# Kernel tuning notes

Measured on AMD Instinct MI355X. Metric: run time of the kernel, lower is better.

## Reference

```python
import jax, jax.numpy as jnp
import numpy as np

N = 8192      # total nodes (128 graphs x 64 electrodes)
L = 256       # signal_length
F = 64        # num_features
H = 128       # hidden_channels
G = 128       # num graphs
E = 262144    # num edges
C = 2         # n_classes


def setup_inputs() -> dict:
    key = jax.random.key(0)
    ks = jax.random.split(key, 20)
    def rn(k, shape, scale=0.05):
        return jax.random.normal(k, shape, jnp.float32) * scale
    return dict(
        x=jax.random.normal(ks[0], (N, L), jnp.float32),
        edge_index=jax.random.randint(ks[1], (2, E), 0, N),
        batch=jnp.repeat(jnp.arange(G), N // G),  # sorted graph id per node
        cw0=rn(ks[2], (F, 1, 7)), cb0=rn(ks[3], (F,)),
        cw_mid=rn(ks[4], (3, F, F, 5)), cb_mid=rn(ks[5], (3, F)),  # convs-2 = 3 middle convs
        cw_last=rn(ks[6], (F, F, 3)), cb_last=rn(ks[7], (F,)),
        enc_w=rn(ks[8], (F, F * 4)), enc_b=rn(ks[9], (F,)),  # in = F*((L-1)//2**6+1) = 256
        g0_rel_w=rn(ks[10], (H, F)), g0_rel_b=rn(ks[11], (H,)), g0_root_w=rn(ks[12], (H, F)),
        g_rel_w=rn(ks[13], (7, H, H)), g_rel_b=rn(ks[14], (7, H)), g_root_w=rn(ks[15], (7, H, H)),
        lin_w=rn(ks[16], (3, H, H)), lin_b=rn(ks[17], (3, H)),
        out_w=rn(ks[18], (C, H)), out_b=rn(ks[19], (C,)),
    )


def _conv1d(x, w, b, stride, pad):
    # x: [N, Cin, L], w: [Cout, Cin, K]
    y = jax.lax.conv_general_dilated(x, w, (stride,), [(pad, pad)],
                                     dimension_numbers=('NCH', 'OIH', 'NCH'))
    return y + b[None, :, None]


def reference(x, edge_index, batch, cw0, cb0, cw_mid, cb_mid, cw_last, cb_last,
              enc_w, enc_b, g0_rel_w, g0_rel_b, g0_root_w,
              g_rel_w, g_rel_b, g_root_w, lin_w, lin_b, out_w, out_b):
    act = jax.nn.relu
    rows = x.shape[0]
    h = x[:, None, :]                                    # [N, 1, L]
    h = act(_conv1d(h, cw0, cb0, 2, 3))                  # [N, F, L/2]
    for i in range(3):                                   # middle convs, k=5 s=2 p=2
        h = act(_conv1d(h, cw_mid[i], cb_mid[i], 2, 2))
    h = act(_conv1d(h, cw_last, cb_last, 2, 1))          # k=3 s=2 p=1 -> [N, F, 8]
    # AvgPool1d(k=3, s=2, p=1), count_include_pad=True -> always divide by 3
    h = jax.lax.reduce_window(h, 0.0, jax.lax.add, (1, 1, 3), (1, 1, 2),
                              [(0, 0), (0, 0), (1, 1)]) / 3.0   # [N, F, 4]
    h = h.reshape(rows, -1)                              # [N, F*4]
    h = h @ enc_w.T + enc_b                              # [N, F]
    src, dst = edge_index[0], edge_index[1]
    def gconv(h, rel_w, rel_b, root_w):
        # PyG GraphConv (aggr='add'): lin_rel(sum_j x_j) + lin_root(x)
        agg = jax.ops.segment_sum(h[src], dst, num_segments=N)
        return agg @ rel_w.T + rel_b + h @ root_w.T
    h = act(gconv(h, g0_rel_w, g0_rel_b, g0_root_w))     # hop 0: F -> H
    for i in range(7):                                   # hops 1..7: H -> H
        h = act(gconv(h, g_rel_w[i], g_rel_b[i], g_root_w[i]))
    # global mean pool by graph id
    sums = jax.ops.segment_sum(h, batch, num_segments=G)
    cnt = jax.ops.segment_sum(jnp.ones((N, 1), h.dtype), batch, num_segments=G)
    h = sums / jnp.maximum(cnt, 1.0)                     # [G, H]
    for i in range(3):
        h = act(h @ lin_w[i].T + lin_b[i])
    logits = h @ out_w.T + out_b                         # [G, C]
    return jax.nn.log_softmax(logits, -1)
```

## Files before the change

kernel.cpp:

```cpp
#include <hip/hip_runtime.h>
#include <hip/hip_bf16.h>

#define DEV_INLINE __device__ __forceinline__

typedef _Float16 f16;
typedef _Float16 f16x4 __attribute__((ext_vector_type(4)));
typedef _Float16 f16x8 __attribute__((ext_vector_type(8)));
typedef __bf16 bf16;
typedef __bf16 bf16x8 __attribute__((ext_vector_type(8)));
typedef float f32x16 __attribute__((ext_vector_type(16)));
typedef float f32x4 __attribute__((ext_vector_type(4)));

constexpr int N_NODES = 8192;
constexpr int G = 128;
constexpr int E_EDGES = 262144;


template<int MT, int LOG_PN, int IN_PS, int OUT_PS>
DEV_INLINE void conv_mid(const f16* __restrict__ wb, const float* __restrict__ bias,
                         char* inb, char* outb, int w, int l) {
  const int cht = w & 1;
  const int o_lane = cht * 32 + (l & 31);
  const int khalf = l >> 5;
  if ((w >> 1) < MT) {
    f16x8 wf[5][4];
#pragma unroll
    for (int k = 0; k < 5; k++)
#pragma unroll
      for (int s = 0; s < 4; s++)
        wf[k][s] = *(const f16x8*)&wb[(k * 64 + o_lane) * 64 + s * 16 + khalf * 8];
    f32x16 binit;
#pragma unroll
    for (int g = 0; g < 4; g++) {
      const float4 b4 = *(const float4*)&bias[cht * 32 + 8 * g + khalf * 4];
      binit[4 * g + 0] = b4.x; binit[4 * g + 1] = b4.y;
      binit[4 * g + 2] = b4.z; binit[4 * g + 3] = b4.w;
    }
    for (int mt = (w >> 1); mt < MT; mt += 2) {
      const int mo = mt * 32 + (l & 31);
      const int node = mo >> LOG_PN;
      const int po = mo & ((1 << LOG_PN) - 1);
      f32x16 acc = binit;
#pragma unroll
      for (int k = 0; k < 5; k++) {
        const int d = k - 2;
        const int par = d & 1;
        const int row = po + (d >> 1) + 1;
        const char* rb = inb + ((node * 2 + par) * IN_PS + row) * 128;
        const int fx = row & 7;
#pragma unroll
        for (int s = 0; s < 4; s++) {
          const int c8 = 2 * s + khalf;
          f16x8 af = *(const f16x8*)(rb + ((c8 ^ fx) << 4));
          acc = __builtin_amdgcn_mfma_f32_32x32x16_f16(wf[k][s], af, acc, 0, 0, 0);
        }
      }
      const int orow = (po >> 1) + 1;
      const int ofx = orow & 7;
      char* base = outb + ((node * 2 + (po & 1)) * OUT_PS + orow) * 128 + khalf * 8;
#pragma unroll
      for (int g = 0; g < 4; g++) {
        f16x4 h4;
        h4[0] = (f16)fmaxf(acc[4 * g + 0], 0.f);
        h4[1] = (f16)fmaxf(acc[4 * g + 1], 0.f);
        h4[2] = (f16)fmaxf(acc[4 * g + 2], 0.f);
        h4[3] = (f16)fmaxf(acc[4 * g + 3], 0.f);
        *(f16x4*)(base + (((cht * 4 + g) ^ ofx) << 4)) = h4;
      }
    }
  }
}

struct alignas(16) L12LDS {
  union {
    char act1[2][2][66][128];
    char a2s[16384];
  } A;
  f16 xs16[2][272];
};

__global__ __launch_bounds__(256)
__attribute__((amdgpu_waves_per_eu(4, 4)))
void conv_l1l2_kernel(
    const float* __restrict__ x,
    const f16* __restrict__ w0f, const float* __restrict__ cb0,
    const f16* __restrict__ wbmid, const float* __restrict__ cb_mid,
    f16* __restrict__ a2g) {
  __shared__ L12LDS lds;
  const int tid = threadIdx.x;
  const int w = tid >> 6, l = tid & 63;
  const int n0 = blockIdx.x * 2;

  for (int idx = tid; idx < 512; idx += 256) {
    int node = idx >> 8, j = idx & 255;
    lds.xs16[node][3 + j] = (f16)x[(size_t)(n0 + node) * 256 + j];
  }
  if (tid < 64) {
    int node = tid >> 5, t = tid & 31;
    int par = (t >> 3) & 1, hi = t >> 4, j = t & 7;
    *(int4*)&lds.A.act1[node][par][hi ? 65 : 0][j * 16] = make_int4(0, 0, 0, 0);
  } else if (tid < 96) {
    int t3 = tid - 64;
    int node = t3 >> 4, s = t3 & 15;
    int slot = (s < 3) ? s : (256 + s);
    lds.xs16[node][slot] = (f16)0.f;
  }
  __syncthreads();

  {
    const int cht = w & 1;
    const int o_lane = cht * 32 + (l & 31);
    const int khalf = l >> 5;
    const f16x8 w0frag = *(const f16x8*)&w0f[o_lane * 16 + khalf * 8];
    f32x16 binit;
#pragma unroll
    for (int g = 0; g < 4; g++) {
      const float4 b4 = *(const float4*)&cb0[cht * 32 + 8 * g + khalf * 4];
      binit[4 * g + 0] = b4.x; binit[4 * g + 1] = b4.y;
      binit[4 * g + 2] = b4.z; binit[4 * g + 3] = b4.w;
    }
    for (int mt = (w >> 1); mt < 8; mt += 2) {
      const int mo = mt * 32 + (l & 31);
      const int node = mo >> 7;
      const int po = mo & 127;
      union { uint u[4]; f16x8 v; } au;
      const char* ap = (const char*)&lds.xs16[node][2 * po + khalf * 8];
#pragma unroll
      for (int j = 0; j < 4; j++) au.u[j] = *(const uint*)(ap + 4 * j);
      f32x16 acc = __builtin_amdgcn_mfma_f32_32x32x16_f16(w0frag, au.v, binit, 0, 0, 0);
      const int orow = (po >> 1) + 1;
      const int ofx = orow & 7;
      char* base = (char*)lds.A.act1 + ((node * 2 + (po & 1)) * 66 + orow) * 128 + khalf * 8;
#pragma unroll
      for (int g = 0; g < 4; g++) {
        f16x4 h4;
        h4[0] = (f16)fmaxf(acc[4 * g + 0], 0.f);
        h4[1] = (f16)fmaxf(acc[4 * g + 1], 0.f);
        h4[2] = (f16)fmaxf(acc[4 * g + 2], 0.f);
        h4[3] = (f16)fmaxf(acc[4 * g + 3], 0.f);
        *(f16x4*)(base + (((cht * 4 + g) ^ ofx) << 4)) = h4;
      }
    }
  }
  __syncthreads();

  {
    const int cht = w & 1;
    const int o_lane = cht * 32 + (l & 31);
    const int khalf = l >> 5;
    f16x8 wf[5][4];
#pragma unroll
    for (int k = 0; k < 5; k++)
#pragma unroll
      for (int s = 0; s < 4; s++)
        wf[k][s] = *(const f16x8*)&wbmid[(k * 64 + o_lane) * 64 + s * 16 + khalf * 8];
    f32x16 binit;
#pragma unroll
    for (int g = 0; g < 4; g++) {
      const float4 b4 = *(const float4*)&cb_mid[cht * 32 + 8 * g + khalf * 4];
      binit[4 * g + 0] = b4.x; binit[4 * g + 1] = b4.y;
      binit[4 * g + 2] = b4.z; binit[4 * g + 3] = b4.w;
    }
    f16x4 outv[2][4];
#pragma unroll
    for (int it = 0; it < 2; it++) {
      const int mt = (w >> 1) + it * 2;
      const int mo = mt * 32 + (l & 31);
      const int node = mo >> 6;
      const int po = mo & 63;
      f32x16 acc = binit;
#pragma unroll
      for (int k = 0; k < 5; k++) {
        const int d = k - 2;
        const int par = d & 1;
        const int row = po + (d >> 1) + 1;
        const char* rb = (char*)lds.A.act1 + ((node * 2 + par) * 66 + row) * 128;
        const int fx = row & 7;
#pragma unroll
        for (int s = 0; s < 4; s++) {
          const int c8 = 2 * s + khalf;
          f16x8 af = *(const f16x8*)(rb + ((c8 ^ fx) << 4));
          acc = __builtin_amdgcn_mfma_f32_32x32x16_f16(wf[k][s], af, acc, 0, 0, 0);
        }
      }
#pragma unroll
      for (int g = 0; g < 4; g++) {
        outv[it][g][0] = (f16)fmaxf(acc[4 * g + 0], 0.f);
        outv[it][g][1] = (f16)fmaxf(acc[4 * g + 1], 0.f);
        outv[it][g][2] = (f16)fmaxf(acc[4 * g + 2], 0.f);
        outv[it][g][3] = (f16)fmaxf(acc[4 * g + 3], 0.f);
      }
    }
    __syncthreads();
#pragma unroll
    for (int it = 0; it < 2; it++) {
      const int mt = (w >> 1) + it * 2;
      const int row = mt * 32 + (l & 31);
      char* base = lds.A.a2s + row * 128 + khalf * 8;
#pragma unroll
      for (int g = 0; g < 4; g++)
        *(f16x4*)(base + (((cht * 4 + g) ^ (row & 7)) << 4)) = outv[it][g];
    }
    __syncthreads();
    char* gout = (char*)a2g + (size_t)n0 * 8192;
#pragma unroll
    for (int i = 0; i < 4; i++) {
      const int idx = tid + i * 256;
      const int row = idx >> 3, s = idx & 7;
      int4 v = *(const int4*)(lds.A.a2s + row * 128 + ((s ^ (row & 7)) << 4));
      *(int4*)(gout + idx * 16) = v;
    }
  }
}

struct alignas(16) L3LDS {
  union {
    char in2[2][2][34][128];
    struct {
      float act5[16][68];
      float pooled[2][256];
      float encred[2][2][64];
    } t;
  } U;
  char act3[2][2][18][128];
  char act4[2][2][10][128];
};

__global__ __launch_bounds__(256)
__attribute__((amdgpu_waves_per_eu(4, 4)))
void conv_l3tail_kernel(
    const f16* __restrict__ a2g,
    const f16* __restrict__ wbmid, const float* __restrict__ cb_mid,
    const f16* __restrict__ wb5, const float* __restrict__ cb_last,
    const f16* __restrict__ enc_w16, const float* __restrict__ enc_b,
    float* __restrict__ henc) {
  __shared__ L3LDS lds;
  const int tid = threadIdx.x;
  const int w = tid >> 6, l = tid & 63;
  const int n0 = blockIdx.x * 2;

#pragma unroll
  for (int i = 0; i < 4; i++) {
    const int idx = tid + i * 256;
    const int node = idx >> 9;
    const int rem = idx & 511;
    const int p = rem >> 3, s8 = rem & 7;
    const int row = (p >> 1) + 1, par = p & 1;
    int4 v = *(const int4*)&a2g[((size_t)(n0 + node) * 64 + p) * 64 + s8 * 8];
    *(int4*)((char*)lds.U.in2 + ((node * 2 + par) * 34 + row) * 128
             + ((s8 ^ (row & 7)) << 4)) = v;
  }
  if (tid < 192) {
    int which = tid >> 6;
    int t = tid & 63;
    int node = t >> 5, tt = t & 31;
    int par = (tt >> 3) & 1, hi = tt >> 4, j = tt & 7;
    if (which == 0)
      *(int4*)&lds.U.in2[node][par][hi ? 33 : 0][j * 16] = make_int4(0, 0, 0, 0);
    else if (which == 1)
      *(int4*)&lds.act3[node][par][hi ? 17 : 0][j * 16] = make_int4(0, 0, 0, 0);
    else
      *(int4*)&lds.act4[node][par][hi ? 9 : 0][j * 16] = make_int4(0, 0, 0, 0);
  }
  __syncthreads();

  conv_mid<2, 5, 34, 18>(wbmid + 5 * 64 * 64, cb_mid + 64,
                         (char*)lds.U.in2, (char*)lds.act3, w, l);
  __syncthreads();
  conv_mid<1, 4, 18, 10>(wbmid + 2 * 5 * 64 * 64, cb_mid + 128,
                         (char*)lds.act3, (char*)lds.act4, w, l);
  __syncthreads();

  {
    const int ch_row = w * 16 + (l & 15);
    const int kq = l >> 4;
    f16x8 wf5[3][2];
#pragma unroll
    for (int k = 0; k < 3; k++)
#pragma unroll
      for (int s = 0; s < 2; s++)
        wf5[k][s] = *(const f16x8*)&wb5[(k * 64 + ch_row) * 64 + s * 32 + kq * 8];
    const float4 b4 = *(const float4*)&cb_last[w * 16 + kq * 4];
    f32x4 acc5 = {b4.x, b4.y, b4.z, b4.w};
    const int m5 = l & 15, nd5 = m5 >> 3, p5 = m5 & 7;
#pragma unroll
    for (int k = 0; k < 3; k++) {
      const int d = k - 1;
      const int par = d & 1;
      const int row = p5 + (d >> 1) + 1;
      const char* rb = (char*)lds.act4 + ((nd5 * 2 + par) * 10 + row) * 128;
      const int fx = row & 7;
#pragma unroll
      for (int s = 0; s < 2; s++) {
        const int c8 = 4 * s + kq;
        f16x8 af = *(const f16x8*)(rb + ((c8 ^ fx) << 4));
        acc5 = __builtin_amdgcn_mfma_f32_16x16x32_f16(wf5[k][s], af, acc5, 0, 0, 0);
      }
    }
    f32x4 o4;
    o4[0] = fmaxf(acc5[0], 0.f);
    o4[1] = fmaxf(acc5[1], 0.f);
    o4[2] = fmaxf(acc5[2], 0.f);
    o4[3] = fmaxf(acc5[3], 0.f);
    *(f32x4*)&lds.U.t.act5[nd5 * 8 + p5][w * 16 + kq * 4] = o4;
  }
  __syncthreads();

  for (int jj = tid; jj < 512; jj += 256) {
    int node = jj >> 8, j = jj & 255;
    int c = j >> 2, q = j & 3;
    const float* a5 = &lds.U.t.act5[node * 8][0];
    float v = a5[(2 * q) * 68 + c] + a5[(2 * q + 1) * 68 + c];
    if (q > 0) v += a5[(2 * q - 1) * 68 + c];
    lds.U.t.pooled[node][j] = v * (1.f / 3.f);
  }
  __syncthreads();

  {
    const int node = tid >> 7, tt = tid & 127;
    const int o = tt & 63, jg = tt >> 6;
    float acc = 0.f;
    const f16x8* ew = (const f16x8*)&enc_w16[o * 256 + jg * 128];
    const float4* pj = (const float4*)&lds.U.t.pooled[node][jg * 128];
#pragma unroll 4
    for (int j8 = 0; j8 < 16; j8++) {
      f16x8 e8 = ew[j8];
      float4 p0 = pj[2 * j8], p1 = pj[2 * j8 + 1];
      acc += (float)e8[0] * p0.x + (float)e8[1] * p0.y +
             (float)e8[2] * p0.z + (float)e8[3] * p0.w +
             (float)e8[4] * p1.x + (float)e8[5] * p1.y +
             (float)e8[6] * p1.z + (float)e8[7] * p1.w;
    }
    lds.U.t.encred[node][jg][o] = acc;
  }
  __syncthreads();
  if (tid < 128) {
    int node = tid >> 6, o = tid & 63;
    henc[(size_t)(n0 + node) * 64 + o] =
        lds.U.t.encred[node][0][o] + lds.U.t.encred[node][1][o] + enc_b[o];
  }
}

__global__ void wprep_all(const float* __restrict__ cw0,
                          const float* __restrict__ cw_mid, const float* __restrict__ cw_last,
                          const float* __restrict__ enc_w,
                          const float* __restrict__ g0_rel, const float* __restrict__ g0_root,
                          const float* __restrict__ g0_rel_b,
                          const float* __restrict__ g_rel, const float* __restrict__ g_root,
                          const float* __restrict__ g_rel_b,
                          f16* __restrict__ w0f, f16* __restrict__ wbmid, f16* __restrict__ wb5,
                          f16* __restrict__ enc_w16,
                          bf16* __restrict__ wg, float* __restrict__ bg) {
  int idx = blockIdx.x * 256 + threadIdx.x;
  if (idx < 64 * 16) {
    int o = idx >> 4, k = idx & 15;
    w0f[idx] = (k < 7) ? (f16)cw0[o * 7 + k] : (f16)0.f;
  }
  if (idx < 3 * 5 * 64 * 64) {
    int lay = idx / (5 * 64 * 64);
    int rem = idx % (5 * 64 * 64);
    int k = rem / 4096;
    int o = (rem >> 6) & 63;
    int c = rem & 63;
    wbmid[idx] = (f16)cw_mid[((lay * 64 + o) * 64 + c) * 5 + k];
  } else {
    int i2 = idx - 3 * 5 * 64 * 64;
    if (i2 < 3 * 64 * 64) {
      int k = i2 / 4096;
      int o = (i2 >> 6) & 63;
      int c = i2 & 63;
      wb5[i2] = (f16)cw_last[(o * 64 + c) * 3 + k];
    }
  }
  if (idx < 64 * 256) enc_w16[idx] = (f16)enc_w[idx];
  if (idx < 128 * 128) {
    int o = idx >> 7, k = idx & 127;
    float v = (k < 64) ? g0_rel[o * 64 + k] : g0_root[o * 64 + (k - 64)];
    bf16 h = (bf16)v;
    wg[idx] = h;
    wg[128 * 128 + idx] = (bf16)(v - (float)h);
  }
  if (idx < 7 * 128 * 256) {
    int lsel = idx / (128 * 256);
    int r = idx % (128 * 256);
    int o = r >> 8, k = r & 255;
    float v = (k < 128) ? g_rel[(lsel * 128 + o) * 128 + k]
                        : g_root[(lsel * 128 + o) * 128 + (k - 128)];
    bf16 h = (bf16)v;
    size_t base = 2 * 128 * 128 + (size_t)lsel * 2 * 128 * 256;
    wg[base + r] = h;
    wg[base + 128 * 256 + r] = (bf16)(v - (float)h);
  }
  if (idx < 8 * 128) {
    int lsel = idx >> 7, o = idx & 127;
    bg[idx] = (lsel == 0) ? g0_rel_b[o] : g_rel_b[(lsel - 1) * 128 + o];
  }
}

__global__ void hist_kernel(const int* __restrict__ dst, int* __restrict__ cnt) {
  int e = blockIdx.x * 256 + threadIdx.x;
  atomicAdd(&cnt[dst[e]], 1);
}

__global__ void scan_kernel(const int* __restrict__ cnt, int* __restrict__ rp) {
  __shared__ int part[256];
  int t = threadIdx.x;
  int base = t * 32;
  int local[32];
  int s = 0;
#pragma unroll
  for (int i = 0; i < 32; i++) { local[i] = cnt[base + i]; s += local[i]; }
  part[t] = s;
  __syncthreads();
  for (int off = 1; off < 256; off <<= 1) {
    int v = (t >= off) ? part[t - off] : 0;
    __syncthreads();
    part[t] += v;
    __syncthreads();
  }
  int run = part[t] - s;
#pragma unroll
  for (int i = 0; i < 32; i++) { rp[base + i] = run; run += local[i]; }
  if (t == 255) rp[N_NODES] = run;
}

__global__ void fill_kernel(const int* __restrict__ src, const int* __restrict__ dst,
                            const int* __restrict__ rp, int* __restrict__ cur,
                            int* __restrict__ csr) {
  int e = blockIdx.x * 256 + threadIdx.x;
  int r = dst[e];
  int p = atomicAdd(&cur[r], 1);
  csr[rp[r] + p] = src[e];
}

template<int D>
__global__ __launch_bounds__(256) void gatherf(
    const float* __restrict__ h, const int* __restrict__ csr,
    const int* __restrict__ rp, float* __restrict__ agg) {
  constexpr int LPN = D / 4;
  const int node = blockIdx.x * (256 / LPN) + (threadIdx.x / LPN);
  const int cl = threadIdx.x & (LPN - 1);
  const int s = rp[node], e = rp[node + 1];
  float4 a0 = make_float4(0.f, 0.f, 0.f, 0.f);
  float4 a1 = make_float4(0.f, 0.f, 0.f, 0.f);
  float4 a2 = make_float4(0.f, 0.f, 0.f, 0.f);
  float4 a3 = make_float4(0.f, 0.f, 0.f, 0.f);
  int i = s;
  for (; i + 3 < e; i += 4) {
    const int m0 = csr[i], m1 = csr[i + 1], m2 = csr[i + 2], m3 = csr[i + 3];
    float4 v0 = *(const float4*)&h[(size_t)m0 * D + cl * 4];
    float4 v1 = *(const float4*)&h[(size_t)m1 * D + cl * 4];
    float4 v2 = *(const float4*)&h[(size_t)m2 * D + cl * 4];
    float4 v3 = *(const float4*)&h[(size_t)m3 * D + cl * 4];
    a0.x += v0.x; a0.y += v0.y; a0.z += v0.z; a0.w += v0.w;
    a1.x += v1.x; a1.y += v1.y; a1.z += v1.z; a1.w += v1.w;
    a2.x += v2.x; a2.y += v2.y; a2.z += v2.z; a2.w += v2.w;
    a3.x += v3.x; a3.y += v3.y; a3.z += v3.z; a3.w += v3.w;
  }
  for (; i < e; i++) {
    const int m0 = csr[i];
    float4 v0 = *(const float4*)&h[(size_t)m0 * D + cl * 4];
    a0.x += v0.x; a0.y += v0.y; a0.z += v0.z; a0.w += v0.w;
  }
  a0.x += a1.x + a2.x + a3.x;
  a0.y += a1.y + a2.y + a3.y;
  a0.z += a1.z + a2.z + a3.z;
  a0.w += a1.w + a2.w + a3.w;
  *(float4*)&agg[(size_t)node * D + cl * 4] = a0;
}

template<int K>
__global__ __launch_bounds__(256) void gnn_gemm_bf(
    const float* __restrict__ agg, const float* __restrict__ hroot,
    const bf16* __restrict__ wg, const float* __restrict__ bg,
    float* __restrict__ hout) {
  constexpr int F = K / 2;
  constexpr int ROWB = K * 2;
  constexpr int KSTEPS = K / 16;
  __shared__ alignas(16) char smem[2][32 * K * 2];
  const int tid = threadIdx.x;
  const int l = tid & 63, w = tid >> 6;
  const int n0 = blockIdx.x * 32;

  {
    const int row = tid >> 3, p = tid & 7;
    constexpr int cpp = K / 64;
#pragma unroll
    for (int j = 0; j < cpp; j++) {
      const int slot = p * cpp + j;
      const int c0 = slot * 8;
      const float* src = (c0 < F) ? &agg[(size_t)(n0 + row) * F + c0]
                                  : &hroot[(size_t)(n0 + row) * F + (c0 - F)];
      float4 v0 = ((const float4*)src)[0];
      float4 v1 = ((const float4*)src)[1];
      float vv[8] = {v0.x, v0.y, v0.z, v0.w, v1.x, v1.y, v1.z, v1.w};
      bf16x8 hi8, lo8;
#pragma unroll
      for (int e = 0; e < 8; e++) {
        float v = vv[e];
        bf16 h = (bf16)v;
        hi8[e] = h;
        lo8[e] = (bf16)(v - (float)h);
      }
      const int off = row * ROWB + ((slot ^ (row & 7)) << 4);
      *(bf16x8*)(smem[0] + off) = hi8;
      *(bf16x8*)(smem[1] + off) = lo8;
    }
  }

  const int ch = w * 32 + (l & 31);
  const int khalf = l >> 5;
  bf16x8 whi[KSTEPS], wlo[KSTEPS];
  const bf16* wrow = wg + (size_t)ch * K + khalf * 8;
#pragma unroll
  for (int ks = 0; ks < KSTEPS; ks++) {
    whi[ks] = *(const bf16x8*)&wrow[ks * 16];
    wlo[ks] = *(const bf16x8*)&wrow[128 * K + ks * 16];
  }
  const float bv = bg[ch];

  __syncthreads();

  const int row0 = l & 31;
  f32x16 acc = {0,0,0,0,0,0,0,0,0,0,0,0,0,0,0,0};
#pragma unroll
  for (int ks = 0; ks < KSTEPS; ks++) {
    const int slot = ks * 2 + khalf;
    const int off = row0 * ROWB + ((slot ^ (row0 & 7)) << 4);
    bf16x8 ah = *(const bf16x8*)(smem[0] + off);
    bf16x8 al = *(const bf16x8*)(smem[1] + off);
    acc = __builtin_amdgcn_mfma_f32_32x32x16_bf16(ah, whi[ks], acc, 0, 0, 0);
    acc = __builtin_amdgcn_mfma_f32_32x32x16_bf16(al, whi[ks], acc, 0, 0, 0);
    acc = __builtin_amdgcn_mfma_f32_32x32x16_bf16(ah, wlo[ks], acc, 0, 0, 0);
  }

#pragma unroll
  for (int r = 0; r < 16; r++) {
    const int nl = (r & 3) + 8 * (r >> 2) + 4 * khalf;
    hout[(size_t)(n0 + nl) * 128 + ch] = fmaxf(acc[r] + bv, 0.f);
  }
}

__global__ __launch_bounds__(256) void poolg(const float* __restrict__ h,
                                             float* __restrict__ pooled) {
  const int g = blockIdx.x;
  const int tid = threadIdx.x;
  const int ch = tid & 127, half = tid >> 7;
  const float* base = h + ((size_t)g * 64 + half * 32) * 128 + ch;
  float s = 0.f;
#pragma unroll 8
  for (int i = 0; i < 32; i++) s += base[(size_t)i * 128];
  __shared__ float red[256];
  red[tid] = s;
  __syncthreads();
  if (tid < 128) pooled[(size_t)g * 128 + tid] = (red[tid] + red[tid + 128]) * (1.f / 64.f);
}

__global__ __launch_bounds__(128) void mlp_kernel(
    const float* __restrict__ pooled,
    const float* __restrict__ lin_w, const float* __restrict__ lin_b,
    const float* __restrict__ out_w, const float* __restrict__ out_b,
    float* __restrict__ out) {
  const int g = blockIdx.x;
  const int t = threadIdx.x;
  __shared__ float hs[128];
  __shared__ float lg[2];
  hs[t] = pooled[(size_t)g * 128 + t];
  __syncthreads();
  for (int lsel = 0; lsel < 3; lsel++) {
    float acc = lin_b[lsel * 128 + t];
    for (int j = 0; j < 128; j++) acc += hs[j] * lin_w[(lsel * 128 + t) * 128 + j];
    __syncthreads();
    hs[t] = fmaxf(acc, 0.f);
    __syncthreads();
  }
  if (t < 2) {
    float acc = out_b[t];
    for (int j = 0; j < 128; j++) acc += hs[j] * out_w[t * 128 + j];
    lg[t] = acc;
  }
  __syncthreads();
  if (t < 2) {
    float m = fmaxf(lg[0], lg[1]);
    float lse = m + logf(expf(lg[0] - m) + expf(lg[1] - m));
    out[g * 2 + t] = lg[t] - lse;
  }
}

extern "C" void kernel_launch(void* const* d_in, const int* in_sizes, int n_in,
                              void* d_out, int out_size, void* d_ws, size_t ws_size,
                              hipStream_t stream) {
  const float* x       = (const float*)d_in[0];
  const int*   edge    = (const int*)d_in[1];
  const float* cw0     = (const float*)d_in[3];
  const float* cb0     = (const float*)d_in[4];
  const float* cw_mid  = (const float*)d_in[5];
  const float* cb_mid  = (const float*)d_in[6];
  const float* cw_last = (const float*)d_in[7];
  const float* cb_last = (const float*)d_in[8];
  const float* enc_w   = (const float*)d_in[9];
  const float* enc_b   = (const float*)d_in[10];
  const float* g0_rel_w  = (const float*)d_in[11];
  const float* g0_rel_b  = (const float*)d_in[12];
  const float* g0_root_w = (const float*)d_in[13];
  const float* g_rel_w   = (const float*)d_in[14];
  const float* g_rel_b   = (const float*)d_in[15];
  const float* g_root_w  = (const float*)d_in[16];
  const float* lin_w     = (const float*)d_in[17];
  const float* lin_b     = (const float*)d_in[18];
  const float* out_w     = (const float*)d_in[19];
  const float* out_b     = (const float*)d_in[20];
  float* out = (float*)d_out;

  const int* esrc = edge;
  const int* edst = edge + E_EDGES;

  char* ws = (char*)d_ws;
  size_t off = 0;
  auto alloc = [&](size_t bytes) {
    void* p = ws + off;
    off += (bytes + 255) & ~size_t(255);
    return p;
  };
  float* henc = (float*)alloc((size_t)N_NODES * 64 * 4);
  float* hA   = (float*)alloc((size_t)N_NODES * 128 * 4);
  float* hB   = (float*)alloc((size_t)N_NODES * 128 * 4);
  float* agg  = (float*)alloc((size_t)N_NODES * 128 * 4);
  bf16* wg    = (bf16*)alloc((size_t)(128 * 128 + 7 * 128 * 256) * 2 * 2);
  float* bg   = (float*)alloc((size_t)8 * 128 * 4);
  float* pooled = (float*)alloc((size_t)G * 128 * 4);
  int* cnt  = (int*)alloc((size_t)N_NODES * 4);
  int* rp   = (int*)alloc((size_t)(N_NODES + 1) * 4);
  int* cur  = (int*)alloc((size_t)N_NODES * 4);
  int* csr  = (int*)alloc((size_t)E_EDGES * 4);
  f16* w0f   = (f16*)alloc((size_t)64 * 16 * 2);
  f16* wbmid = (f16*)alloc((size_t)3 * 5 * 64 * 64 * 2);
  f16* wb5   = (f16*)alloc((size_t)3 * 64 * 64 * 2);
  f16* enc_w16 = (f16*)alloc((size_t)64 * 256 * 2);
  f16* a2g   = (f16*)alloc((size_t)N_NODES * 64 * 64 * 2);

  hipMemsetAsync(cnt, 0, (size_t)N_NODES * 4, stream);
  hipMemsetAsync(cur, 0, (size_t)N_NODES * 4, stream);

  wprep_all<<<896, 256, 0, stream>>>(cw0, cw_mid, cw_last, enc_w,
                                     g0_rel_w, g0_root_w, g0_rel_b,
                                     g_rel_w, g_root_w, g_rel_b,
                                     w0f, wbmid, wb5, enc_w16, wg, bg);
  conv_l1l2_kernel<<<N_NODES / 2, 256, 0, stream>>>(x, w0f, cb0, wbmid, cb_mid, a2g);
  conv_l3tail_kernel<<<N_NODES / 2, 256, 0, stream>>>(
      a2g, wbmid, cb_mid, wb5, cb_last, enc_w16, enc_b, henc);

  hist_kernel<<<E_EDGES / 256, 256, 0, stream>>>(edst, cnt);
  scan_kernel<<<1, 256, 0, stream>>>(cnt, rp);
  fill_kernel<<<E_EDGES / 256, 256, 0, stream>>>(esrc, edst, rp, cur, csr);

  gatherf<64><<<N_NODES / 16, 256, 0, stream>>>(henc, csr, rp, agg);
  gnn_gemm_bf<128><<<N_NODES / 32, 256, 0, stream>>>(agg, henc, wg, bg, hA);

  float* hprev = hA;
  float* hnext = hB;
  for (int lsel = 0; lsel < 7; lsel++) {
    gatherf<128><<<N_NODES / 8, 256, 0, stream>>>(hprev, csr, rp, agg);
    gnn_gemm_bf<256><<<N_NODES / 32, 256, 0, stream>>>(
        agg, hprev, wg + 2 * 128 * 128 + (size_t)lsel * 2 * 128 * 256,
        bg + (lsel + 1) * 128, hnext);
    float* tmp = hprev; hprev = hnext; hnext = tmp;
  }

  poolg<<<G, 256, 0, stream>>>(hprev, pooled);
  mlp_kernel<<<G, 128, 0, stream>>>(pooled, lin_w, lin_b, out_w, out_b, out);
}
```

Before: 373.0 us.

## Restructure conv tail to one node per wave with wave-local LDS

```diff
diff --git a/kernel.cpp b/kernel.cpp
--- a/kernel.cpp
+++ b/kernel.cpp
@@ -15,61 +15,7 @@
 constexpr int G = 128;
 constexpr int E_EDGES = 262144;
 
-
-template<int MT, int LOG_PN, int IN_PS, int OUT_PS>
-DEV_INLINE void conv_mid(const f16* __restrict__ wb, const float* __restrict__ bias,
-                         char* inb, char* outb, int w, int l) {
-  const int cht = w & 1;
-  const int o_lane = cht * 32 + (l & 31);
-  const int khalf = l >> 5;
-  if ((w >> 1) < MT) {
-    f16x8 wf[5][4];
-#pragma unroll
-    for (int k = 0; k < 5; k++)
-#pragma unroll
-      for (int s = 0; s < 4; s++)
-        wf[k][s] = *(const f16x8*)&wb[(k * 64 + o_lane) * 64 + s * 16 + khalf * 8];
-    f32x16 binit;
-#pragma unroll
-    for (int g = 0; g < 4; g++) {
-      const float4 b4 = *(const float4*)&bias[cht * 32 + 8 * g + khalf * 4];
-      binit[4 * g + 0] = b4.x; binit[4 * g + 1] = b4.y;
-      binit[4 * g + 2] = b4.z; binit[4 * g + 3] = b4.w;
-    }
-    for (int mt = (w >> 1); mt < MT; mt += 2) {
-      const int mo = mt * 32 + (l & 31);
-      const int node = mo >> LOG_PN;
-      const int po = mo & ((1 << LOG_PN) - 1);
-      f32x16 acc = binit;
-#pragma unroll
-      for (int k = 0; k < 5; k++) {
-        const int d = k - 2;
-        const int par = d & 1;
-        const int row = po + (d >> 1) + 1;
-        const char* rb = inb + ((node * 2 + par) * IN_PS + row) * 128;
-        const int fx = row & 7;
-#pragma unroll
-        for (int s = 0; s < 4; s++) {
-          const int c8 = 2 * s + khalf;
-          f16x8 af = *(const f16x8*)(rb + ((c8 ^ fx) << 4));
-          acc = __builtin_amdgcn_mfma_f32_32x32x16_f16(wf[k][s], af, acc, 0, 0, 0);
-        }
-      }
-      const int orow = (po >> 1) + 1;
-      const int ofx = orow & 7;
-      char* base = outb + ((node * 2 + (po & 1)) * OUT_PS + orow) * 128 + khalf * 8;
-#pragma unroll
-      for (int g = 0; g < 4; g++) {
-        f16x4 h4;
-        h4[0] = (f16)fmaxf(acc[4 * g + 0], 0.f);
-        h4[1] = (f16)fmaxf(acc[4 * g + 1], 0.f);
-        h4[2] = (f16)fmaxf(acc[4 * g + 2], 0.f);
-        h4[3] = (f16)fmaxf(acc[4 * g + 3], 0.f);
-        *(f16x4*)(base + (((cht * 4 + g) ^ ofx) << 4)) = h4;
-      }
-    }
-  }
-}
+#define LDS_FENCE() asm volatile("s_waitcnt lgkmcnt(0)" ::: "memory")
 
 struct alignas(16) L12LDS {
   union {
@@ -79,9 +25,7 @@
   f16 xs16[2][272];
 };
 
-__global__ __launch_bounds__(256)
-__attribute__((amdgpu_waves_per_eu(4, 4)))
-void conv_l1l2_kernel(
+__global__ __launch_bounds__(256, 4) void conv_l1l2_kernel(
     const float* __restrict__ x,
     const f16* __restrict__ w0f, const float* __restrict__ cb0,
     const f16* __restrict__ wbmid, const float* __restrict__ cb_mid,
@@ -99,11 +43,13 @@
     int node = tid >> 5, t = tid & 31;
     int par = (t >> 3) & 1, hi = t >> 4, j = t & 7;
     *(int4*)&lds.A.act1[node][par][hi ? 65 : 0][j * 16] = make_int4(0, 0, 0, 0);
-  } else if (tid < 96) {
+  } else if (tid < 128) {
     int t3 = tid - 64;
-    int node = t3 >> 4, s = t3 & 15;
-    int slot = (s < 3) ? s : (256 + s);
-    lds.xs16[node][slot] = (f16)0.f;
+    if (t3 < 32) {
+      int node = t3 >> 4, s = t3 & 15;
+      int slot = (s < 3) ? s : (256 + s);
+      lds.xs16[node][slot] = (f16)0.f;
+    }
   }
   __syncthreads();
 
@@ -213,131 +159,180 @@
   }
 }
 
-struct alignas(16) L3LDS {
-  union {
-    char in2[2][2][34][128];
-    struct {
-      float act5[16][68];
-      float pooled[2][256];
-      float encred[2][2][64];
-    } t;
-  } U;
-  char act3[2][2][18][128];
-  char act4[2][2][10][128];
+struct alignas(16) TailLDS {
+  struct alignas(16) {
+    char act3[32][128];
+    char act4[16][128];
+    float act5[8][68];
+    float pooled[256];
+  } wv[4];
 };
 
-__global__ __launch_bounds__(256)
-__attribute__((amdgpu_waves_per_eu(4, 4)))
-void conv_l3tail_kernel(
+__global__ __launch_bounds__(256) void conv_tail_wave(
     const f16* __restrict__ a2g,
     const f16* __restrict__ wbmid, const float* __restrict__ cb_mid,
     const f16* __restrict__ wb5, const float* __restrict__ cb_last,
     const f16* __restrict__ enc_w16, const float* __restrict__ enc_b,
     float* __restrict__ henc) {
-  __shared__ L3LDS lds;
-  const int tid = threadIdx.x;
-  const int w = tid >> 6, l = tid & 63;
-  const int n0 = blockIdx.x * 2;
-
-#pragma unroll
-  for (int i = 0; i < 4; i++) {
-    const int idx = tid + i * 256;
-    const int node = idx >> 9;
-    const int rem = idx & 511;
-    const int p = rem >> 3, s8 = rem & 7;
-    const int row = (p >> 1) + 1, par = p & 1;
-    int4 v = *(const int4*)&a2g[((size_t)(n0 + node) * 64 + p) * 64 + s8 * 8];
-    *(int4*)((char*)lds.U.in2 + ((node * 2 + par) * 34 + row) * 128
-             + ((s8 ^ (row & 7)) << 4)) = v;
-  }
-  if (tid < 192) {
-    int which = tid >> 6;
-    int t = tid & 63;
-    int node = t >> 5, tt = t & 31;
-    int par = (tt >> 3) & 1, hi = tt >> 4, j = tt & 7;
-    if (which == 0)
-      *(int4*)&lds.U.in2[node][par][hi ? 33 : 0][j * 16] = make_int4(0, 0, 0, 0);
-    else if (which == 1)
-      *(int4*)&lds.act3[node][par][hi ? 17 : 0][j * 16] = make_int4(0, 0, 0, 0);
-    else
-      *(int4*)&lds.act4[node][par][hi ? 9 : 0][j * 16] = make_int4(0, 0, 0, 0);
-  }
-  __syncthreads();
-
-  conv_mid<2, 5, 34, 18>(wbmid + 5 * 64 * 64, cb_mid + 64,
-                         (char*)lds.U.in2, (char*)lds.act3, w, l);
-  __syncthreads();
-  conv_mid<1, 4, 18, 10>(wbmid + 2 * 5 * 64 * 64, cb_mid + 128,
-                         (char*)lds.act3, (char*)lds.act4, w, l);
-  __syncthreads();
-
-  {
-    const int ch_row = w * 16 + (l & 15);
-    const int kq = l >> 4;
-    f16x8 wf5[3][2];
-#pragma unroll
-    for (int k = 0; k < 3; k++)
-#pragma unroll
-      for (int s = 0; s < 2; s++)
-        wf5[k][s] = *(const f16x8*)&wb5[(k * 64 + ch_row) * 64 + s * 32 + kq * 8];
-    const float4 b4 = *(const float4*)&cb_last[w * 16 + kq * 4];
-    f32x4 acc5 = {b4.x, b4.y, b4.z, b4.w};
-    const int m5 = l & 15, nd5 = m5 >> 3, p5 = m5 & 7;
+  __shared__ TailLDS lds;
+  const int w = threadIdx.x >> 6, l = threadIdx.x & 63;
+  const int n = blockIdx.x * 4 + w;
+  auto& mb = lds.wv[w];
+  const int p16 = l & 15;
+  const int kq = l >> 4;
+
+  const f16* wL3 = wbmid + 5 * 64 * 64;
+  const f16* wL4 = wbmid + 2 * 5 * 64 * 64;
+
+  {
+    f32x4 acc[2][4];
+#pragma unroll
+    for (int ct = 0; ct < 4; ct++) {
+      const float4 b4 = *(const float4*)&cb_mid[64 + ct * 16 + kq * 4];
+      acc[0][ct][0] = b4.x; acc[0][ct][1] = b4.y; acc[0][ct][2] = b4.z; acc[0][ct][3] = b4.w;
+      acc[1][ct] = acc[0][ct];
+    }
+    const f16 zero8v = (f16)0.f;
+#pragma unroll
+    for (int k = 0; k < 5; k++) {
+#pragma unroll
+      for (int ks = 0; ks < 2; ks++) {
+        f16x8 b0 = {zero8v,zero8v,zero8v,zero8v,zero8v,zero8v,zero8v,zero8v};
+        f16x8 b1 = b0;
+        {
+          const int ip0 = 2 * p16 + k - 2;
+          if ((unsigned)ip0 < 64u)
+            b0 = *(const f16x8*)&a2g[((size_t)n * 64 + ip0) * 64 + ks * 32 + kq * 8];
+          const int ip1 = 2 * (16 + p16) + k - 2;
+          if ((unsigned)ip1 < 64u)
+            b1 = *(const f16x8*)&a2g[((size_t)n * 64 + ip1) * 64 + ks * 32 + kq * 8];
+        }
+#pragma unroll
+        for (int ct = 0; ct < 4; ct++) {
+          f16x8 wv8 = *(const f16x8*)&wL3[(k * 64 + ct * 16 + p16) * 64 + ks * 32 + kq * 8];
+          acc[0][ct] = __builtin_amdgcn_mfma_f32_16x16x32_f16(wv8, b0, acc[0][ct], 0, 0, 0);
+          acc[1][ct] = __builtin_amdgcn_mfma_f32_16x16x32_f16(wv8, b1, acc[1][ct], 0, 0, 0);
+        }
+      }
+    }
+#pragma unroll
+    for (int pt = 0; pt < 2; pt++) {
+      const int p = pt * 16 + p16;
+#pragma unroll
+      for (int ct = 0; ct < 4; ct++) {
+        f16x4 h4;
+        h4[0] = (f16)fmaxf(acc[pt][ct][0], 0.f);
+        h4[1] = (f16)fmaxf(acc[pt][ct][1], 0.f);
+        h4[2] = (f16)fmaxf(acc[pt][ct][2], 0.f);
+        h4[3] = (f16)fmaxf(acc[pt][ct][3], 0.f);
+        const int slot = ct * 2 + (kq >> 1);
+        *(f16x4*)((char*)mb.act3 + p * 128 + ((slot ^ (p & 7)) << 4) + (kq & 1) * 8) = h4;
+      }
+    }
+  }
+  LDS_FENCE();
+
+  {
+    f32x4 acc[4];
+#pragma unroll
+    for (int ct = 0; ct < 4; ct++) {
+      const float4 b4 = *(const float4*)&cb_mid[128 + ct * 16 + kq * 4];
+      acc[ct][0] = b4.x; acc[ct][1] = b4.y; acc[ct][2] = b4.z; acc[ct][3] = b4.w;
+    }
+#pragma unroll
+    for (int k = 0; k < 5; k++) {
+#pragma unroll
+      for (int ks = 0; ks < 2; ks++) {
+        const int ip = 2 * p16 + k - 2;
+        f16x8 b0 = {(f16)0.f,(f16)0.f,(f16)0.f,(f16)0.f,(f16)0.f,(f16)0.f,(f16)0.f,(f16)0.f};
+        if ((unsigned)ip < 32u) {
+          const int slot = ks * 4 + kq;
+          b0 = *(const f16x8*)((char*)mb.act3 + ip * 128 + ((slot ^ (ip & 7)) << 4));
+        }
+#pragma unroll
+        for (int ct = 0; ct < 4; ct++) {
+          f16x8 wv8 = *(const f16x8*)&wL4[(k * 64 + ct * 16 + p16) * 64 + ks * 32 + kq * 8];
+          acc[ct] = __builtin_amdgcn_mfma_f32_16x16x32_f16(wv8, b0, acc[ct], 0, 0, 0);
+        }
+      }
+    }
+    const int p = p16;
+#pragma unroll
+    for (int ct = 0; ct < 4; ct++) {
+      f16x4 h4;
+      h4[0] = (f16)fmaxf(acc[ct][0], 0.f);
+      h4[1] = (f16)fmaxf(acc[ct][1], 0.f);
+      h4[2] = (f16)fmaxf(acc[ct][2], 0.f);
+      h4[3] = (f16)fmaxf(acc[ct][3], 0.f);
+      const int slot = ct * 2 + (kq >> 1);
+      *(f16x4*)((char*)mb.act4 + p * 128 + ((slot ^ (p & 7)) << 4) + (kq & 1) * 8) = h4;
+    }
+  }
+  LDS_FENCE();
+
+  {
+    f32x4 acc[4];
+#pragma unroll
+    for (int ct = 0; ct < 4; ct++) {
+      const float4 b4 = *(const float4*)&cb_last[ct * 16 + kq * 4];
+      acc[ct][0] = b4.x; acc[ct][1] = b4.y; acc[ct][2] = b4.z; acc[ct][3] = b4.w;
+    }
 #pragma unroll
     for (int k = 0; k < 3; k++) {
-      const int d = k - 1;
-      const int par = d & 1;
-      const int row = p5 + (d >> 1) + 1;
-      const char* rb = (char*)lds.act4 + ((nd5 * 2 + par) * 10 + row) * 128;
-      const int fx = row & 7;
-#pragma unroll
-      for (int s = 0; s < 2; s++) {
-        const int c8 = 4 * s + kq;
-        f16x8 af = *(const f16x8*)(rb + ((c8 ^ fx) << 4));
-        acc5 = __builtin_amdgcn_mfma_f32_16x16x32_f16(wf5[k][s], af, acc5, 0, 0, 0);
-      }
-    }
-    f32x4 o4;
-    o4[0] = fmaxf(acc5[0], 0.f);
-    o4[1] = fmaxf(acc5[1], 0.f);
-    o4[2] = fmaxf(acc5[2], 0.f);
-    o4[3] = fmaxf(acc5[3], 0.f);
-    *(f32x4*)&lds.U.t.act5[nd5 * 8 + p5][w * 16 + kq * 4] = o4;
-  }
-  __syncthreads();
-
-  for (int jj = tid; jj < 512; jj += 256) {
-    int node = jj >> 8, j = jj & 255;
-    int c = j >> 2, q = j & 3;
-    const float* a5 = &lds.U.t.act5[node * 8][0];
-    float v = a5[(2 * q) * 68 + c] + a5[(2 * q + 1) * 68 + c];
-    if (q > 0) v += a5[(2 * q - 1) * 68 + c];
-    lds.U.t.pooled[node][j] = v * (1.f / 3.f);
-  }
-  __syncthreads();
-
-  {
-    const int node = tid >> 7, tt = tid & 127;
-    const int o = tt & 63, jg = tt >> 6;
+#pragma unroll
+      for (int ks = 0; ks < 2; ks++) {
+        const int ip = 2 * p16 + k - 1;
+        f16x8 b0 = {(f16)0.f,(f16)0.f,(f16)0.f,(f16)0.f,(f16)0.f,(f16)0.f,(f16)0.f,(f16)0.f};
+        if ((unsigned)ip < 16u) {
+          const int slot = ks * 4 + kq;
+          b0 = *(const f16x8*)((char*)mb.act4 + ip * 128 + ((slot ^ (ip & 7)) << 4));
+        }
+#pragma unroll
+        for (int ct = 0; ct < 4; ct++) {
+          f16x8 wv8 = *(const f16x8*)&wb5[(k * 64 + ct * 16 + p16) * 64 + ks * 32 + kq * 8];
+          acc[ct] = __builtin_amdgcn_mfma_f32_16x16x32_f16(wv8, b0, acc[ct], 0, 0, 0);
+        }
+      }
+    }
+    if (p16 < 8) {
+#pragma unroll
+      for (int ct = 0; ct < 4; ct++) {
+        f32x4 o4;
+        o4[0] = fmaxf(acc[ct][0], 0.f);
+        o4[1] = fmaxf(acc[ct][1], 0.f);
+        o4[2] = fmaxf(acc[ct][2], 0.f);
+        o4[3] = fmaxf(acc[ct][3], 0.f);
+        *(f32x4*)&mb.act5[p16][ct * 16 + kq * 4] = o4;
+      }
+    }
+  }
+  LDS_FENCE();
+
+  {
+    const int c = l;
+#pragma unroll
+    for (int q = 0; q < 4; q++) {
+      float v = mb.act5[2 * q][c] + mb.act5[2 * q + 1][c];
+      if (q > 0) v += mb.act5[2 * q - 1][c];
+      mb.pooled[c * 4 + q] = v * (1.f / 3.f);
+    }
+  }
+  LDS_FENCE();
+
+  {
+    const int o = l;
     float acc = 0.f;
-    const f16x8* ew = (const f16x8*)&enc_w16[o * 256 + jg * 128];
-    const float4* pj = (const float4*)&lds.U.t.pooled[node][jg * 128];
+    const f16x8* ew = (const f16x8*)&enc_w16[o * 256];
 #pragma unroll 4
-    for (int j8 = 0; j8 < 16; j8++) {
+    for (int j8 = 0; j8 < 32; j8++) {
       f16x8 e8 = ew[j8];
-      float4 p0 = pj[2 * j8], p1 = pj[2 * j8 + 1];
-      acc += (float)e8[0] * p0.x + (float)e8[1] * p0.y +
-             (float)e8[2] * p0.z + (float)e8[3] * p0.w +
-             (float)e8[4] * p1.x + (float)e8[5] * p1.y +
-             (float)e8[6] * p1.z + (float)e8[7] * p1.w;
-    }
-    lds.U.t.encred[node][jg][o] = acc;
-  }
-  __syncthreads();
-  if (tid < 128) {
-    int node = tid >> 6, o = tid & 63;
-    henc[(size_t)(n0 + node) * 64 + o] =
-        lds.U.t.encred[node][0][o] + lds.U.t.encred[node][1][o] + enc_b[o];
+      const float* pj = &mb.pooled[j8 * 8];
+      acc += (float)e8[0] * pj[0] + (float)e8[1] * pj[1] +
+             (float)e8[2] * pj[2] + (float)e8[3] * pj[3] +
+             (float)e8[4] * pj[4] + (float)e8[5] * pj[5] +
+             (float)e8[6] * pj[6] + (float)e8[7] * pj[7];
+    }
+    henc[(size_t)n * 64 + o] = acc + enc_b[o];
   }
 }
 
@@ -647,7 +642,7 @@
                                      g_rel_w, g_root_w, g_rel_b,
                                      w0f, wbmid, wb5, enc_w16, wg, bg);
   conv_l1l2_kernel<<<N_NODES / 2, 256, 0, stream>>>(x, w0f, cb0, wbmid, cb_mid, a2g);
-  conv_l3tail_kernel<<<N_NODES / 2, 256, 0, stream>>>(
+  conv_tail_wave<<<N_NODES / 4, 256, 0, stream>>>(
       a2g, wbmid, cb_mid, wb5, cb_last, enc_w16, enc_b, henc);
 
   hist_kernel<<<E_EDGES / 256, 256, 0, stream>>>(edst, cnt);
```

After: 429.2 us. 15.1% more time.
